# Performance work log

Hardware: AMD Instinct MI355X
Metric: run time of the kernel (lower is better)

## Reference

```python
import jax, jax.numpy as jnp
import numpy as np

B, S, H = 32, 4096, 512
N = 2 * H  # n = hidden_size * 2


def setup_inputs() -> dict:
    key = jax.random.key(0)
    ks = jax.random.split(key, 10)
    scale = 1.0 / np.sqrt(N)
    return {
        "dec_in_state": jax.random.normal(ks[0], (B, N), jnp.float32),
        "enc_states": jax.random.normal(ks[1], (B, S, N), jnp.float32),
        "enc_lens": jax.random.randint(ks[2], (B,), 1, S + 1),
        "coverage_vector": jax.random.uniform(ks[3], (B, S), jnp.float32),
        "Wh": jax.random.normal(ks[4], (N, N), jnp.float32) * scale,
        "bh": jnp.zeros((N,), jnp.float32),
        "Ws": jax.random.normal(ks[5], (N, N), jnp.float32) * scale,
        "bs": jnp.zeros((N,), jnp.float32),
        "wc": jax.random.normal(ks[6], (N,), jnp.float32) * scale,  # W_c: Linear(1, N, bias=False)
        "v": jax.random.normal(ks[7], (N,), jnp.float32) * scale,   # v: Linear(N, 1, bias=False)
    }


def reference(dec_in_state, enc_states, enc_lens, coverage_vector, Wh, bh, Ws, bs, wc, v):
    seq_len = enc_states.shape[1]
    # additive Bahdanau features: [B,S,N]
    enc_feats = jnp.einsum("bsn,mn->bsm", enc_states, Wh) + bh
    dec_feats = dec_in_state @ Ws.T + bs  # [B,N]
    cov_feats = coverage_vector[..., None] * wc  # [B,S,N] (Linear(1,N,no bias))
    e = jnp.tanh(enc_feats + dec_feats[:, None, :] + cov_feats) @ v  # [B,S]
    # masked renormalized softmax
    mask = (jnp.arange(seq_len)[None, :] < enc_lens[:, None]).astype(e.dtype)  # [B,S]
    attn = jax.nn.softmax(e, axis=1) * mask
    attn = attn / attn.sum(axis=1, keepdims=True)
    context = jnp.einsum("bs,bsn->bn", attn, enc_states)  # [B,N]
    coverage_out = coverage_vector + attn
    return (context, attn, coverage_out)
```

## Files before the change

kernel.cpp:

```cpp
#include <hip/hip_runtime.h>
#include <math.h>

#define B 32
#define S 4096
#define N 1024

typedef short short8 __attribute__((ext_vector_type(8)));
typedef short short4v __attribute__((ext_vector_type(4)));
typedef float float4v __attribute__((ext_vector_type(4)));

__device__ inline short f2bf(float f) {
    unsigned u = __builtin_bit_cast(unsigned, f);
    u += 0x7fffu + ((u >> 16) & 1u);
    return (short)(u >> 16);
}

__device__ __forceinline__ void load_lds16(const void* g, void* l) {
    __builtin_amdgcn_global_load_lds(
        (const __attribute__((address_space(1))) void*)g,
        (__attribute__((address_space(3))) void*)l, 16, 0, 0);
}

__global__ __launch_bounds__(256)
void prep_kernel(const float* __restrict__ dec, const float* __restrict__ Ws,
                 const float* __restrict__ bs, float* __restrict__ dec_feats,
                 float* __restrict__ e) {
    int tg = blockIdx.x * 256 + threadIdx.x;
    if (tg < B * S) e[tg] = 0.f;

    int wid  = (blockIdx.x << 2) + (threadIdx.x >> 6);
    int lane = threadIdx.x & 63;
    int m = wid >> 5, b = wid & 31;
    const float4* drow = (const float4*)(dec + (size_t)b * N);
    const float4* wrow = (const float4*)(Ws + (size_t)m * N);
    float acc = 0.f;
#pragma unroll
    for (int k = 0; k < 4; ++k) {
        float4 a = drow[lane + (k << 6)];
        float4 w = wrow[lane + (k << 6)];
        acc += a.x * w.x + a.y * w.y + a.z * w.z + a.w * w.w;
    }
    acc += __shfl_xor(acc, 1);  acc += __shfl_xor(acc, 2);
    acc += __shfl_xor(acc, 4);  acc += __shfl_xor(acc, 8);
    acc += __shfl_xor(acc, 16); acc += __shfl_xor(acc, 32);
    if (lane == 0) dec_feats[(size_t)b * N + m] = acc + bs[m];
}

__global__ __launch_bounds__(256)
void cvt_bf16_kernel(const float* __restrict__ enc, short* __restrict__ encb,
                     const float* __restrict__ Wh, short* __restrict__ whb) {
    size_t i0 = (size_t)blockIdx.x * 256 + threadIdx.x;
    size_t stride = (size_t)gridDim.x * 256;
    const size_t n8e = (size_t)B * S * N / 8;
    for (size_t i = i0; i < n8e; i += stride) {
        const float4v* s = (const float4v*)(enc + i * 8);
        float4v a = s[0], b = s[1];
        short8 o = { f2bf(a.x), f2bf(a.y), f2bf(a.z), f2bf(a.w),
                     f2bf(b.x), f2bf(b.y), f2bf(b.z), f2bf(b.w) };
        *(short8*)(encb + i * 8) = o;
    }
    const size_t n8w = (size_t)N * N / 8;
    for (size_t i = i0; i < n8w; i += stride) {
        const float4v* s = (const float4v*)(Wh + i * 8);
        float4v a = s[0], b = s[1];
        short8 o = { f2bf(a.x), f2bf(a.y), f2bf(a.z), f2bf(a.w),
                     f2bf(b.x), f2bf(b.y), f2bf(b.z), f2bf(b.w) };
        *(short8*)(whb + i * 8) = o;
    }
}

#define REGION_A(slot, hk) ((slot)*16384 + (hk)*8192)
#define REGION_B(slot, hk) (32768 + (slot)*16384 + (hk)*8192)

__global__ __launch_bounds__(512, 2)
void score_mfma8_kernel(const short* __restrict__ encb, const short* __restrict__ whb,
                        const float* __restrict__ bh, const float* __restrict__ dec_feats,
                        const float* __restrict__ cov, const float* __restrict__ wc,
                        const float* __restrict__ v, float* __restrict__ e) {
    __shared__ short lds[65536];

    unsigned bid = blockIdx.x;
    unsigned c = (bid & 7u) * 256u + (bid >> 3);
    int rt = (int)(c >> 2), mtile = (int)(c & 3u);
    int r0 = rt * 256, m0 = mtile * 256;

    int t = threadIdx.x, lane = t & 63, w = t >> 6;
    int wm_ = w >> 2, wn_ = w & 3;
    int cq = lane >> 4, cm = lane & 15;

    int srow = lane >> 2;
    int sg = (lane & 3) ^ ((lane >> 3) & 3);
    const short* aS0 = encb + (size_t)(r0 + w * 16 + srow) * N + sg * 8;
    const short* aS1 = aS0 + (size_t)128 * N;
    const short* bS0 = whb + (size_t)(m0 + w * 16 + srow) * N + sg * 8;
    const short* bS1 = bS0 + (size_t)128 * N;
    const int dc0 = w * 512, dc1 = dc0 + 4096;

    int aoff[8], boff[4];
#pragma unroll
    for (int f = 0; f < 8; ++f) {
        int R = wm_ * 128 + f * 16 + cm;
        aoff[f] = R * 32 + ((cq ^ ((R >> 1) & 3)) << 3);
    }
#pragma unroll
    for (int j = 0; j < 4; ++j) {
        int R = wn_ * 64 + j * 16 + cm;
        boff[j] = R * 32 + ((cq ^ ((R >> 1) & 3)) << 3);
    }

    float4v acc[8][4];
#pragma unroll
    for (int f = 0; f < 8; ++f)
#pragma unroll
        for (int j = 0; j < 4; ++j) acc[f][j] = (float4v){0.f, 0.f, 0.f, 0.f};

#define STAGE(srcp0, srcp1, region, colElem) do {                         \
        int _cc = (colElem) & (N - 1);                                    \
        load_lds16((srcp0) + _cc, &lds[(region) + dc0]);                  \
        load_lds16((srcp1) + _cc, &lds[(region) + dc1]);                  \
    } while (0)

    STAGE(aS0, aS1, REGION_A(0, 0), 0);
    STAGE(bS0, bS1, REGION_B(0, 0), 0);
    STAGE(aS0, aS1, REGION_A(0, 1), 32);
    STAGE(bS0, bS1, REGION_B(0, 1), 32);
    STAGE(aS0, aS1, REGION_A(1, 0), 64);
    STAGE(bS0, bS1, REGION_B(1, 0), 64);
    asm volatile("s_waitcnt vmcnt(8)" ::: "memory");
    __builtin_amdgcn_s_barrier();

    short8 bf[4];

#define PHASE(slot, sub, SRC0, SRC1, SREGION, SCOL) do {                      \
        const int hk_ = (sub) >> 1, mh_ = (sub) & 1;                          \
        if (mh_ == 0) {                                                       \
            _Pragma("unroll")                                                 \
            for (int j = 0; j < 4; ++j)                                       \
                bf[j] = *(const short8*)&lds[REGION_B(slot, hk_) + boff[j]];  \
        }                                                                     \
        short8 af[4];                                                         \
        _Pragma("unroll")                                                     \
        for (int f = 0; f < 4; ++f)                                           \
            af[f] = *(const short8*)&lds[REGION_A(slot, hk_) + aoff[mh_ * 4 + f]]; \
        STAGE(SRC0, SRC1, SREGION, SCOL);                                     \
        __builtin_amdgcn_s_barrier();                                         \
        asm volatile("s_waitcnt lgkmcnt(0)" ::: "memory");                    \
        __builtin_amdgcn_sched_barrier(0);                                    \
        __builtin_amdgcn_s_setprio(1);                                        \
        _Pragma("unroll")                                                     \
        for (int f = 0; f < 4; ++f)                                           \
            _Pragma("unroll")                                                 \
            for (int j = 0; j < 4; ++j)                                       \
                acc[mh_ * 4 + f][j] = __builtin_amdgcn_mfma_f32_16x16x32_bf16(\
                    af[f], bf[j], acc[mh_ * 4 + f][j], 0, 0, 0);              \
        __builtin_amdgcn_s_setprio(0);                                        \
        if (mh_ == 1) asm volatile("s_waitcnt vmcnt(8)" ::: "memory");        \
        __builtin_amdgcn_s_barrier();                                         \
    } while (0)

#pragma unroll 1
    for (int i = 0; i < 8; ++i) {
        int kb = i * 128;
        PHASE(0, 0, aS0, aS1, REGION_A(1, 1), kb + 96);
        PHASE(0, 1, bS0, bS1, REGION_B(1, 1), kb + 96);
        PHASE(0, 2, aS0, aS1, REGION_A(0, 0), kb + 128);
        PHASE(0, 3, bS0, bS1, REGION_B(0, 0), kb + 128);
        PHASE(1, 0, aS0, aS1, REGION_A(0, 1), kb + 160);
        PHASE(1, 1, bS0, bS1, REGION_B(0, 1), kb + 160);
        PHASE(1, 2, aS0, aS1, REGION_A(1, 0), kb + 192);
        PHASE(1, 3, bS0, bS1, REGION_B(1, 0), kb + 192);
    }
    asm volatile("s_waitcnt vmcnt(0)" ::: "memory");
#undef PHASE
#undef STAGE

    int bidx = r0 >> 12;
    const float* df = dec_feats + ((size_t)bidx << 10);

    float basej[4], wcj[4], vj[4];
#pragma unroll
    for (int j = 0; j < 4; ++j) {
        int m = m0 + wn_ * 64 + j * 16 + cm;
        basej[j] = bh[m] + df[m];
        wcj[j]   = wc[m];
        vj[j]    = v[m];
    }

#pragma unroll
    for (int f = 0; f < 8; ++f) {
        int rbase = r0 + wm_ * 128 + f * 16 + cq * 4;
        float4v cvv = *(const float4v*)&cov[rbase];
        float cv[4] = {cvv.x, cvv.y, cvv.z, cvv.w};
        float rs[4] = {0.f, 0.f, 0.f, 0.f};
#pragma unroll
        for (int j = 0; j < 4; ++j) {
#pragma unroll
            for (int reg = 0; reg < 4; ++reg) {
                float val = acc[f][j][reg] + basej[j] + cv[reg] * wcj[j];
                val = fminf(fmaxf(val, -15.f), 15.f);
                float t2 = __builtin_amdgcn_exp2f(val * 2.8853900817779268f);
                float r  = __builtin_amdgcn_rcpf(t2 + 1.f);
                float th = fmaf(-2.f, r, 1.f);
                rs[reg] = fmaf(th, vj[j], rs[reg]);
            }
        }
#pragma unroll
        for (int reg = 0; reg < 4; ++reg) {
            float p = rs[reg];
            p += __shfl_xor(p, 1);
            p += __shfl_xor(p, 2);
            p += __shfl_xor(p, 4);
            p += __shfl_xor(p, 8);
            if (cm == 0) atomicAdd(&e[rbase + reg], p);
        }
    }
}

#define BR 128
#define BM 128
#define BK 64
#define LDK (BK + 8)

__global__ __launch_bounds__(256)
void score_mfma_kernel(const float* __restrict__ enc, const float* __restrict__ Wh,
                       const float* __restrict__ bh, const float* __restrict__ dec_feats,
                       const float* __restrict__ cov, const float* __restrict__ wc,
                       const float* __restrict__ v, float* __restrict__ e) {
    __shared__ short As[BR][LDK];
    __shared__ short Bs[BM][LDK];

    unsigned h   = blockIdx.x;
    unsigned xcd = h & 7u;
    unsigned mt  = (h >> 3) & 7u;
    unsigned g   = h >> 6;
    int r0 = (int)(xcd + 8u * g) * BR;
    int m0 = (int)mt * BM;

    int t    = threadIdx.x;
    int lane = t & 63;
    int w    = t >> 6;
    int wr   = (w >> 1) * 64;
    int wm   = (w & 1) * 64;
    int cq   = lane >> 4;
    int cm   = lane & 15;

    float4v acc[4][4];
#pragma unroll
    for (int i = 0; i < 4; ++i)
#pragma unroll
        for (int j = 0; j < 4; ++j) acc[i][j] = (float4v){0.f, 0.f, 0.f, 0.f};

    int srow = t >> 4;
    int scol = (t & 15) * 4;

    for (int k0 = 0; k0 < N; k0 += BK) {
#pragma unroll
        for (int p = 0; p < 8; ++p) {
            int row = p * 16 + srow;
            float4v a = *(const float4v*)(enc + (size_t)(r0 + row) * N + k0 + scol);
            short4v ap = { f2bf(a.x), f2bf(a.y), f2bf(a.z), f2bf(a.w) };
            *(short4v*)&As[row][scol] = ap;
            float4v bq = *(const float4v*)(Wh + (size_t)(m0 + row) * N + k0 + scol);
            short4v bp = { f2bf(bq.x), f2bf(bq.y), f2bf(bq.z), f2bf(bq.w) };
            *(short4v*)&Bs[row][scol] = bp;
        }
        __syncthreads();
#pragma unroll
        for (int ks = 0; ks < BK; ks += 32) {
            short8 af[4], bfr[4];
#pragma unroll
            for (int i = 0; i < 4; ++i)
                af[i] = *(const short8*)&As[wr + i * 16 + cm][ks + cq * 8];
#pragma unroll
            for (int j = 0; j < 4; ++j)
                bfr[j] = *(const short8*)&Bs[wm + j * 16 + cm][ks + cq * 8];
#pragma unroll
            for (int i = 0; i < 4; ++i)
#pragma unroll
                for (int j = 0; j < 4; ++j)
                    acc[i][j] = __builtin_amdgcn_mfma_f32_16x16x32_bf16(
                        af[i], bfr[j], acc[i][j], 0, 0, 0);
        }
        __syncthreads();
    }

    int b = r0 >> 12;
    const float* df = dec_feats + ((size_t)b << 10);

    float basej[4], wcj[4], vj[4];
#pragma unroll
    for (int j = 0; j < 4; ++j) {
        int m = m0 + wm + j * 16 + cm;
        basej[j] = bh[m] + df[m];
        wcj[j]   = wc[m];
        vj[j]    = v[m];
    }

#pragma unroll
    for (int i = 0; i < 4; ++i) {
        int rbase = r0 + wr + i * 16 + cq * 4;
        float cv[4];
#pragma unroll
        for (int reg = 0; reg < 4; ++reg) cv[reg] = cov[rbase + reg];
        float rs[4] = {0.f, 0.f, 0.f, 0.f};
#pragma unroll
        for (int j = 0; j < 4; ++j) {
#pragma unroll
            for (int reg = 0; reg < 4; ++reg) {
                float val = acc[i][j][reg] + basej[j] + cv[reg] * wcj[j];
                val = fminf(fmaxf(val, -15.f), 15.f);
                float t2 = __builtin_amdgcn_exp2f(val * 2.8853900817779268f);
                float r  = __builtin_amdgcn_rcpf(t2 + 1.f);
                float th = fmaf(-2.f, r, 1.f);
                rs[reg] = fmaf(th, vj[j], rs[reg]);
            }
        }
#pragma unroll
        for (int reg = 0; reg < 4; ++reg) {
            float p = rs[reg];
            p += __shfl_xor(p, 1);
            p += __shfl_xor(p, 2);
            p += __shfl_xor(p, 4);
            p += __shfl_xor(p, 8);
            if (cm == 0) atomicAdd(&e[rbase + reg], p);
        }
    }
}

__global__ __launch_bounds__(1024)
void softmax_kernel(const float* __restrict__ e, const int* __restrict__ lens,
                    const float* __restrict__ cov,
                    float* __restrict__ attn, float* __restrict__ cov_out) {
    int b = blockIdx.x, t = threadIdx.x;
    int lane = t & 63, wid = t >> 6;
    int len = lens[b];
    const float* eb = e + (size_t)b * S;
    __shared__ float redm[16], reds[16];

    float ev[4];
    float mx = -INFINITY;
#pragma unroll
    for (int k = 0; k < 4; ++k) {
        int s = t + (k << 10);
        ev[k] = (s < len) ? eb[s] : -INFINITY;
        mx = fmaxf(mx, ev[k]);
    }
    mx = fmaxf(mx, __shfl_xor(mx, 1));  mx = fmaxf(mx, __shfl_xor(mx, 2));
    mx = fmaxf(mx, __shfl_xor(mx, 4));  mx = fmaxf(mx, __shfl_xor(mx, 8));
    mx = fmaxf(mx, __shfl_xor(mx, 16)); mx = fmaxf(mx, __shfl_xor(mx, 32));
    if (lane == 0) redm[wid] = mx;
    __syncthreads();
    if (t < 16) {
        float v2 = redm[t];
        v2 = fmaxf(v2, __shfl_xor(v2, 1)); v2 = fmaxf(v2, __shfl_xor(v2, 2));
        v2 = fmaxf(v2, __shfl_xor(v2, 4)); v2 = fmaxf(v2, __shfl_xor(v2, 8));
        if (t == 0) redm[0] = v2;
    }
    __syncthreads();
    mx = redm[0];

    float ex[4];
    float sum = 0.f;
#pragma unroll
    for (int k = 0; k < 4; ++k) {
        ex[k] = exp2f((ev[k] - mx) * 1.4426950408889634f);
        sum += ex[k];
    }
    sum += __shfl_xor(sum, 1);  sum += __shfl_xor(sum, 2);
    sum += __shfl_xor(sum, 4);  sum += __shfl_xor(sum, 8);
    sum += __shfl_xor(sum, 16); sum += __shfl_xor(sum, 32);
    if (lane == 0) reds[wid] = sum;
    __syncthreads();
    if (t < 16) {
        float v2 = reds[t];
        v2 += __shfl_xor(v2, 1); v2 += __shfl_xor(v2, 2);
        v2 += __shfl_xor(v2, 4); v2 += __shfl_xor(v2, 8);
        if (t == 0) reds[0] = v2;
    }
    __syncthreads();
    float inv = 1.f / reds[0];

#pragma unroll
    for (int k = 0; k < 4; ++k) {
        int s = t + (k << 10);
        float a = ex[k] * inv;
        attn[(size_t)b * S + s] = a;
        cov_out[(size_t)b * S + s] = cov[(size_t)b * S + s] + a;
    }
}

#define SCH 64
__global__ __launch_bounds__(256)
void context_part_kernel(const float* __restrict__ attn, const float* __restrict__ enc,
                         float* __restrict__ part) {
    int b  = blockIdx.y;
    int ch = blockIdx.x;
    int s0 = ch * (S / SCH);
    int n4 = threadIdx.x;
    const float4* ep = (const float4*)(enc + ((size_t)b * S + s0) * N);
    float4 acc = {0.f, 0.f, 0.f, 0.f};
    for (int s = 0; s < S / SCH; ++s) {
        float a = attn[(size_t)b * S + s0 + s];
        float4 ev = ep[(size_t)s * (N / 4) + n4];
        acc.x += a * ev.x; acc.y += a * ev.y;
        acc.z += a * ev.z; acc.w += a * ev.w;
    }
    *(float4*)&part[((size_t)b * SCH + ch) * N + n4 * 4] = acc;
}

__global__ __launch_bounds__(256)
void context_reduce_kernel(const float* __restrict__ part, float* __restrict__ ctx) {
    int idx = blockIdx.x * 256 + threadIdx.x;
    int b = idx >> 10, n = idx & (N - 1);
    const float* p = part + (size_t)b * SCH * N + n;
    float acc = 0.f;
#pragma unroll
    for (int c2 = 0; c2 < SCH; ++c2) acc += p[(size_t)c2 * N];
    ctx[idx] = acc;
}

__global__ __launch_bounds__(256)
void context_kernel(const float* __restrict__ attn, const float* __restrict__ enc,
                    float* __restrict__ ctx) {
    int b  = blockIdx.y;
    int s0 = blockIdx.x * (S / SCH);
    int n4 = threadIdx.x;
    const float4* ep = (const float4*)(enc + ((size_t)b * S + s0) * N);
    float4 acc = {0.f, 0.f, 0.f, 0.f};
    for (int s = 0; s < S / SCH; ++s) {
        float a = attn[(size_t)b * S + s0 + s];
        float4 ev = ep[(size_t)s * (N / 4) + n4];
        acc.x += a * ev.x; acc.y += a * ev.y;
        acc.z += a * ev.z; acc.w += a * ev.w;
    }
    float* cp = ctx + (size_t)b * N + n4 * 4;
    atomicAdd(cp + 0, acc.x);
    atomicAdd(cp + 1, acc.y);
    atomicAdd(cp + 2, acc.z);
    atomicAdd(cp + 3, acc.w);
}

extern "C" void kernel_launch(void* const* d_in, const int* in_sizes, int n_in,
                              void* d_out, int out_size, void* d_ws, size_t ws_size,
                              hipStream_t stream) {
    const float* dec  = (const float*)d_in[0];
    const float* enc  = (const float*)d_in[1];
    const int*   lens = (const int*)  d_in[2];
    const float* cov  = (const float*)d_in[3];
    const float* Wh   = (const float*)d_in[4];
    const float* bh   = (const float*)d_in[5];
    const float* Ws   = (const float*)d_in[6];
    const float* bs   = (const float*)d_in[7];
    const float* wc   = (const float*)d_in[8];
    const float* v    = (const float*)d_in[9];

    float* out     = (float*)d_out;
    float* ctx     = out;
    float* attn    = out + (size_t)B * N;
    float* cov_out = attn + (size_t)B * S;

    size_t off_e    = (size_t)B * N * 4;
    size_t off_encb = off_e + (size_t)B * S * 4;
    size_t off_whb  = off_encb + (size_t)B * S * N * 2;
    size_t off_part = off_whb + (size_t)N * N * 2;
    size_t need     = off_part + (size_t)B * SCH * N * 4;

    float* dec_feats = (float*)d_ws;
    float* e         = (float*)((char*)d_ws + off_e);

    prep_kernel<<<8192, 256, 0, stream>>>(dec, Ws, bs, dec_feats, e);

    if (ws_size >= need) {
        short* encb = (short*)((char*)d_ws + off_encb);
        short* whb  = (short*)((char*)d_ws + off_whb);
        float* part = (float*)((char*)d_ws + off_part);
        cvt_bf16_kernel<<<2048, 256, 0, stream>>>(enc, encb, Wh, whb);
        score_mfma8_kernel<<<2048, 512, 0, stream>>>(
            encb, whb, bh, dec_feats, cov, wc, v, e);
        softmax_kernel<<<B, 1024, 0, stream>>>(e, lens, cov, attn, cov_out);
        context_part_kernel<<<dim3(SCH, B), 256, 0, stream>>>(attn, enc, part);
        context_reduce_kernel<<<(B * N) / 256, 256, 0, stream>>>(part, ctx);
    } else {
        hipMemsetAsync(ctx, 0, (size_t)B * N * sizeof(float), stream);
        score_mfma_kernel<<<(B * S / BR) * (N / BM), 256, 0, stream>>>(
            enc, Wh, bh, dec_feats, cov, wc, v, e);
        softmax_kernel<<<B, 1024, 0, stream>>>(e, lens, cov, attn, cov_out);
        context_kernel<<<dim3(SCH, B), 256, 0, stream>>>(attn, enc, ctx);
    }
}
```

Baseline: 1.195 ms.

## Fuse prep and bf16 conversion kernels; process two row tiles per score block

Merges the decoder-feature GEMV, zeroing of e, and the fp32-to-bf16 conversions of enc and Wh into one launch, with block ranges dedicated to each job. The score GEMM kernel now runs half as many blocks, each looping over two consecutive 256-row tiles. The per-column epilogue constants are hoisted out of that loop and loaded once. This removes one kernel launch and amortizes per-block setup, but halves the grid to 1024 blocks, which may leave CUs less evenly loaded.

After: 1.156 ms. -3.3%, faster.

```diff
diff --git a/kernel.cpp b/kernel.cpp
--- a/kernel.cpp
+++ b/kernel.cpp
@@ -19,6 +19,53 @@
     __builtin_amdgcn_global_load_lds(
         (const __attribute__((address_space(1))) void*)g,
         (__attribute__((address_space(3))) void*)l, 16, 0, 0);
+}
+
+__global__ __launch_bounds__(256)
+void prep_cvt_kernel(const float* __restrict__ dec, const float* __restrict__ Ws,
+                     const float* __restrict__ bs, const float* __restrict__ enc,
+                     const float* __restrict__ Wh, float* __restrict__ dec_feats,
+                     float* __restrict__ e, short* __restrict__ encb,
+                     short* __restrict__ whb) {
+    unsigned bid = blockIdx.x;
+    int tid = threadIdx.x;
+    if (bid < 2048u) {
+        if (bid < 512u) e[bid * 256 + tid] = 0.f;
+        const size_t n8e = (size_t)B * S * N / 8;
+        for (size_t i = (size_t)bid * 256 + tid; i < n8e; i += 2048u * 256u) {
+            const float4v* s = (const float4v*)(enc + i * 8);
+            float4v a = s[0], b = s[1];
+            short8 o = { f2bf(a.x), f2bf(a.y), f2bf(a.z), f2bf(a.w),
+                         f2bf(b.x), f2bf(b.y), f2bf(b.z), f2bf(b.w) };
+            *(short8*)(encb + i * 8) = o;
+        }
+    } else if (bid < 2064u) {
+        const size_t n8w = (size_t)N * N / 8;
+        for (size_t i = (size_t)(bid - 2048u) * 256 + tid; i < n8w; i += 16u * 256u) {
+            const float4v* s = (const float4v*)(Wh + i * 8);
+            float4v a = s[0], b = s[1];
+            short8 o = { f2bf(a.x), f2bf(a.y), f2bf(a.z), f2bf(a.w),
+                         f2bf(b.x), f2bf(b.y), f2bf(b.z), f2bf(b.w) };
+            *(short8*)(whb + i * 8) = o;
+        }
+    } else {
+        int wid  = (int)(bid - 2064u) * 4 + (tid >> 6);
+        int lane = tid & 63;
+        int m = wid >> 5, b = wid & 31;
+        const float4* drow = (const float4*)(dec + (size_t)b * N);
+        const float4* wrow = (const float4*)(Ws + (size_t)m * N);
+        float acc = 0.f;
+#pragma unroll
+        for (int k = 0; k < 4; ++k) {
+            float4 a = drow[lane + (k << 6)];
+            float4 w = wrow[lane + (k << 6)];
+            acc += a.x * w.x + a.y * w.y + a.z * w.z + a.w * w.w;
+        }
+        acc += __shfl_xor(acc, 1);  acc += __shfl_xor(acc, 2);
+        acc += __shfl_xor(acc, 4);  acc += __shfl_xor(acc, 8);
+        acc += __shfl_xor(acc, 16); acc += __shfl_xor(acc, 32);
+        if (lane == 0) dec_feats[(size_t)b * N + m] = acc + bs[m];
+    }
 }
 
 __global__ __launch_bounds__(256)
@@ -27,7 +74,6 @@
                  float* __restrict__ e) {
     int tg = blockIdx.x * 256 + threadIdx.x;
     if (tg < B * S) e[tg] = 0.f;
-
     int wid  = (blockIdx.x << 2) + (threadIdx.x >> 6);
     int lane = threadIdx.x & 63;
     int m = wid >> 5, b = wid & 31;
@@ -46,29 +92,6 @@
     if (lane == 0) dec_feats[(size_t)b * N + m] = acc + bs[m];
 }
 
-__global__ __launch_bounds__(256)
-void cvt_bf16_kernel(const float* __restrict__ enc, short* __restrict__ encb,
-                     const float* __restrict__ Wh, short* __restrict__ whb) {
-    size_t i0 = (size_t)blockIdx.x * 256 + threadIdx.x;
-    size_t stride = (size_t)gridDim.x * 256;
-    const size_t n8e = (size_t)B * S * N / 8;
-    for (size_t i = i0; i < n8e; i += stride) {
-        const float4v* s = (const float4v*)(enc + i * 8);
-        float4v a = s[0], b = s[1];
-        short8 o = { f2bf(a.x), f2bf(a.y), f2bf(a.z), f2bf(a.w),
-                     f2bf(b.x), f2bf(b.y), f2bf(b.z), f2bf(b.w) };
-        *(short8*)(encb + i * 8) = o;
-    }
-    const size_t n8w = (size_t)N * N / 8;
-    for (size_t i = i0; i < n8w; i += stride) {
-        const float4v* s = (const float4v*)(Wh + i * 8);
-        float4v a = s[0], b = s[1];
-        short8 o = { f2bf(a.x), f2bf(a.y), f2bf(a.z), f2bf(a.w),
-                     f2bf(b.x), f2bf(b.y), f2bf(b.z), f2bf(b.w) };
-        *(short8*)(whb + i * 8) = o;
-    }
-}
-
 #define REGION_A(slot, hk) ((slot)*16384 + (hk)*8192)
 #define REGION_B(slot, hk) (32768 + (slot)*16384 + (hk)*8192)
 
@@ -80,9 +103,9 @@
     __shared__ short lds[65536];
 
     unsigned bid = blockIdx.x;
-    unsigned c = (bid & 7u) * 256u + (bid >> 3);
-    int rt = (int)(c >> 2), mtile = (int)(c & 3u);
-    int r0 = rt * 256, m0 = mtile * 256;
+    unsigned c = (bid & 7u) * 128u + (bid >> 3);
+    int rtp = (int)(c >> 2), mtile = (int)(c & 3u);
+    int m0 = mtile * 256;
 
     int t = threadIdx.x, lane = t & 63, w = t >> 6;
     int wm_ = w >> 2, wn_ = w & 3;
@@ -90,8 +113,6 @@
 
     int srow = lane >> 2;
     int sg = (lane & 3) ^ ((lane >> 3) & 3);
-    const short* aS0 = encb + (size_t)(r0 + w * 16 + srow) * N + sg * 8;
-    const short* aS1 = aS0 + (size_t)128 * N;
     const short* bS0 = whb + (size_t)(m0 + w * 16 + srow) * N + sg * 8;
     const short* bS1 = bS0 + (size_t)128 * N;
     const int dc0 = w * 512, dc1 = dc0 + 4096;
@@ -108,28 +129,24 @@
         boff[j] = R * 32 + ((cq ^ ((R >> 1) & 3)) << 3);
     }
 
-    float4v acc[8][4];
-#pragma unroll
-    for (int f = 0; f < 8; ++f)
-#pragma unroll
-        for (int j = 0; j < 4; ++j) acc[f][j] = (float4v){0.f, 0.f, 0.f, 0.f};
+    float basej[4], wcj[4], vj[4];
+    {
+        int bidx0 = (rtp * 2 * 256) >> 12;
+        const float* df = dec_feats + ((size_t)bidx0 << 10);
+#pragma unroll
+        for (int j = 0; j < 4; ++j) {
+            int m = m0 + wn_ * 64 + j * 16 + cm;
+            basej[j] = bh[m] + df[m];
+            wcj[j]   = wc[m];
+            vj[j]    = v[m];
+        }
+    }
 
 #define STAGE(srcp0, srcp1, region, colElem) do {                         \
         int _cc = (colElem) & (N - 1);                                    \
         load_lds16((srcp0) + _cc, &lds[(region) + dc0]);                  \
         load_lds16((srcp1) + _cc, &lds[(region) + dc1]);                  \
     } while (0)
-
-    STAGE(aS0, aS1, REGION_A(0, 0), 0);
-    STAGE(bS0, bS1, REGION_B(0, 0), 0);
-    STAGE(aS0, aS1, REGION_A(0, 1), 32);
-    STAGE(bS0, bS1, REGION_B(0, 1), 32);
-    STAGE(aS0, aS1, REGION_A(1, 0), 64);
-    STAGE(bS0, bS1, REGION_B(1, 0), 64);
-    asm volatile("s_waitcnt vmcnt(8)" ::: "memory");
-    __builtin_amdgcn_s_barrier();
-
-    short8 bf[4];
 
 #define PHASE(slot, sub, SRC0, SRC1, SREGION, SCOL) do {                      \
         const int hk_ = (sub) >> 1, mh_ = (sub) & 1;                          \
@@ -159,61 +176,75 @@
     } while (0)
 
 #pragma unroll 1
-    for (int i = 0; i < 8; ++i) {
-        int kb = i * 128;
-        PHASE(0, 0, aS0, aS1, REGION_A(1, 1), kb + 96);
-        PHASE(0, 1, bS0, bS1, REGION_B(1, 1), kb + 96);
-        PHASE(0, 2, aS0, aS1, REGION_A(0, 0), kb + 128);
-        PHASE(0, 3, bS0, bS1, REGION_B(0, 0), kb + 128);
-        PHASE(1, 0, aS0, aS1, REGION_A(0, 1), kb + 160);
-        PHASE(1, 1, bS0, bS1, REGION_B(0, 1), kb + 160);
-        PHASE(1, 2, aS0, aS1, REGION_A(1, 0), kb + 192);
-        PHASE(1, 3, bS0, bS1, REGION_B(1, 0), kb + 192);
-    }
-    asm volatile("s_waitcnt vmcnt(0)" ::: "memory");
+    for (int it = 0; it < 2; ++it) {
+        int r0 = (rtp * 2 + it) * 256;
+        const short* aS0 = encb + (size_t)(r0 + w * 16 + srow) * N + sg * 8;
+        const short* aS1 = aS0 + (size_t)128 * N;
+
+        float4v acc[8][4];
+#pragma unroll
+        for (int f = 0; f < 8; ++f)
+#pragma unroll
+            for (int j = 0; j < 4; ++j) acc[f][j] = (float4v){0.f, 0.f, 0.f, 0.f};
+
+        STAGE(aS0, aS1, REGION_A(0, 0), 0);
+        STAGE(bS0, bS1, REGION_B(0, 0), 0);
+        STAGE(aS0, aS1, REGION_A(0, 1), 32);
+        STAGE(bS0, bS1, REGION_B(0, 1), 32);
+        STAGE(aS0, aS1, REGION_A(1, 0), 64);
+        STAGE(bS0, bS1, REGION_B(1, 0), 64);
+        asm volatile("s_waitcnt vmcnt(8)" ::: "memory");
+        __builtin_amdgcn_s_barrier();
+
+        short8 bf[4];
+
+#pragma unroll 1
+        for (int i = 0; i < 8; ++i) {
+            int kb = i * 128;
+            PHASE(0, 0, aS0, aS1, REGION_A(1, 1), kb + 96);
+            PHASE(0, 1, bS0, bS1, REGION_B(1, 1), kb + 96);
+            PHASE(0, 2, aS0, aS1, REGION_A(0, 0), kb + 128);
+            PHASE(0, 3, bS0, bS1, REGION_B(0, 0), kb + 128);
+            PHASE(1, 0, aS0, aS1, REGION_A(0, 1), kb + 160);
+            PHASE(1, 1, bS0, bS1, REGION_B(0, 1), kb + 160);
+            PHASE(1, 2, aS0, aS1, REGION_A(1, 0), kb + 192);
+            PHASE(1, 3, bS0, bS1, REGION_B(1, 0), kb + 192);
+        }
+        asm volatile("s_waitcnt vmcnt(0)" ::: "memory");
+
+#pragma unroll
+        for (int f = 0; f < 8; ++f) {
+            int rbase = r0 + wm_ * 128 + f * 16 + cq * 4;
+            float4v cvv = *(const float4v*)&cov[rbase];
+            float cv[4] = {cvv.x, cvv.y, cvv.z, cvv.w};
+            float rs[4] = {0.f, 0.f, 0.f, 0.f};
+#pragma unroll
+            for (int j = 0; j < 4; ++j) {
+#pragma unroll
+                for (int reg = 0; reg < 4; ++reg) {
+                    float val = acc[f][j][reg] + basej[j] + cv[reg] * wcj[j];
+                    val = fminf(fmaxf(val, -15.f), 15.f);
+                    float t2 = __builtin_amdgcn_exp2f(val * 2.8853900817779268f);
+                    float r  = __builtin_amdgcn_rcpf(t2 + 1.f);
+                    float th = fmaf(-2.f, r, 1.f);
+                    rs[reg] = fmaf(th, vj[j], rs[reg]);
+                }
+            }
+#pragma unroll
+            for (int reg = 0; reg < 4; ++reg) {
+                float p = rs[reg];
+                p += __shfl_xor(p, 1);
+                p += __shfl_xor(p, 2);
+                p += __shfl_xor(p, 4);
+                p += __shfl_xor(p, 8);
+                if (cm == 0) atomicAdd(&e[rbase + reg], p);
+            }
+        }
+        asm volatile("s_waitcnt vmcnt(0)" ::: "memory");
+        __builtin_amdgcn_s_barrier();
+    }
 #undef PHASE
 #undef STAGE
-
-    int bidx = r0 >> 12;
-    const float* df = dec_feats + ((size_t)bidx << 10);
-
-    float basej[4], wcj[4], vj[4];
-#pragma unroll
-    for (int j = 0; j < 4; ++j) {
-        int m = m0 + wn_ * 64 + j * 16 + cm;
-        basej[j] = bh[m] + df[m];
-        wcj[j]   = wc[m];
-        vj[j]    = v[m];
-    }
-
-#pragma unroll
-    for (int f = 0; f < 8; ++f) {
-        int rbase = r0 + wm_ * 128 + f * 16 + cq * 4;
-        float4v cvv = *(const float4v*)&cov[rbase];
-        float cv[4] = {cvv.x, cvv.y, cvv.z, cvv.w};
-        float rs[4] = {0.f, 0.f, 0.f, 0.f};
-#pragma unroll
-        for (int j = 0; j < 4; ++j) {
-#pragma unroll
-            for (int reg = 0; reg < 4; ++reg) {
-                float val = acc[f][j][reg] + basej[j] + cv[reg] * wcj[j];
-                val = fminf(fmaxf(val, -15.f), 15.f);
-                float t2 = __builtin_amdgcn_exp2f(val * 2.8853900817779268f);
-                float r  = __builtin_amdgcn_rcpf(t2 + 1.f);
-                float th = fmaf(-2.f, r, 1.f);
-                rs[reg] = fmaf(th, vj[j], rs[reg]);
-            }
-        }
-#pragma unroll
-        for (int reg = 0; reg < 4; ++reg) {
-            float p = rs[reg];
-            p += __shfl_xor(p, 1);
-            p += __shfl_xor(p, 2);
-            p += __shfl_xor(p, 4);
-            p += __shfl_xor(p, 8);
-            if (cm == 0) atomicAdd(&e[rbase + reg], p);
-        }
-    }
 }
 
 #define BR 128
@@ -468,19 +499,19 @@
     float* dec_feats = (float*)d_ws;
     float* e         = (float*)((char*)d_ws + off_e);
 
-    prep_kernel<<<8192, 256, 0, stream>>>(dec, Ws, bs, dec_feats, e);
-
     if (ws_size >= need) {
         short* encb = (short*)((char*)d_ws + off_encb);
         short* whb  = (short*)((char*)d_ws + off_whb);
         float* part = (float*)((char*)d_ws + off_part);
-        cvt_bf16_kernel<<<2048, 256, 0, stream>>>(enc, encb, Wh, whb);
-        score_mfma8_kernel<<<2048, 512, 0, stream>>>(
+        prep_cvt_kernel<<<10256, 256, 0, stream>>>(dec, Ws, bs, enc, Wh,
+                                                   dec_feats, e, encb, whb);
+        score_mfma8_kernel<<<1024, 512, 0, stream>>>(
             encb, whb, bh, dec_feats, cov, wc, v, e);
         softmax_kernel<<<B, 1024, 0, stream>>>(e, lens, cov, attn, cov_out);
         context_part_kernel<<<dim3(SCH, B), 256, 0, stream>>>(attn, enc, part);
         context_reduce_kernel<<<(B * N) / 256, 256, 0, stream>>>(part, ctx);
     } else {
+        prep_kernel<<<8192, 256, 0, stream>>>(dec, Ws, bs, dec_feats, e);
         hipMemsetAsync(ctx, 0, (size_t)B * N * sizeof(float), stream);
         score_mfma_kernel<<<(B * S / BR) * (N / BM), 256, 0, stream>>>(
             enc, Wh, bh, dec_feats, cov, wc, v, e);
```
